# Optimization experiments

Measured on AMD Instinct MI355X. Metric: run time of the kernel, lower is better.

The kernel has to match this reference:

```python
import jax, jax.numpy as jnp
import numpy as np

EPS = 1e-8  # matches torch F.cosine_similarity default eps


def setup_inputs() -> dict:
    key = jax.random.key(0)
    k1, k2, k3 = jax.random.split(key, 3)
    B, S, Q, T, D = 1, 5, 512, 64, 2048
    supp = jax.random.normal(k1, (B, S, T, D), dtype=jnp.float32)
    query = jax.random.normal(k2, (B, Q, T, D), dtype=jnp.float32)
    query_ys = jax.random.randint(k3, (Q,), 0, S, dtype=jnp.int64)
    return {"supp": supp, "query": query, "query_ys": query_ys}


def reference(supp, query, query_ys):
    # supp: [B, S, T, D], query: [B, Q, T, D]
    # Pool once over T (mathematically identical to repeat-then-mean).
    sp = supp.mean(axis=-2)   # [B, S, D]
    qp = query.mean(axis=-2)  # [B, Q, D]
    # Pairwise cosine similarity over D -> [B, Q, S]
    num = jnp.einsum('bqd,bsd->bqs', qp, sp)
    qn = jnp.linalg.norm(qp, axis=-1)  # [B, Q]
    sn = jnp.linalg.norm(sp, axis=-1)  # [B, S]
    denom = jnp.maximum(qn[:, :, None] * sn[:, None, :], EPS)
    dist = (num / denom)[0]  # squeeze(0) -> [Q, S]
    # Cross-entropy over the num_supp (class) axis
    logp = jax.nn.log_softmax(dist, axis=-1)
    loss = -jnp.take_along_axis(logp, query_ys[:, None], axis=1).mean()
    return (loss, 1.0 - dist)
```

## Files before the change

### kernel.cpp

```cpp
#include <hip/hip_runtime.h>
#include <hip/hip_bf16.h>

#define S_DIM 5
#define Q_DIM 512
#define T_DIM 64
#define D_DIM 2048
#define EPS_CS 1e-8f

typedef float f32x4 __attribute__((ext_vector_type(4)));

#define WS_SP    0
#define WS_QP    10240
#define WS_NORMS 1058816
#define WS_NLL   1059336

__device__ __forceinline__ float wave_reduce_sum(float v) {
    #pragma unroll
    for (int off = 32; off > 0; off >>= 1)
        v += __shfl_down(v, off, 64);
    return v;
}

__global__ __launch_bounds__(512) void pool_kernel(
    const float* __restrict__ supp, const float* __restrict__ query,
    float* __restrict__ sp, float* __restrict__ qp, float* __restrict__ norms)
{
    const int b   = blockIdx.x;
    const int tid = threadIdx.x;

    const float* src = (b < S_DIM)
        ? supp  + (size_t)b * T_DIM * D_DIM
        : query + (size_t)(b - S_DIM) * T_DIM * D_DIM;
    float* dst = (b < S_DIM)
        ? sp + (size_t)b * D_DIM
        : qp + (size_t)(b - S_DIM) * D_DIM;

    const f32x4* base = (const f32x4*)src;

    f32x4 acc = {0.f, 0.f, 0.f, 0.f};
    #pragma unroll 16
    for (int t = 0; t < T_DIM; ++t) {
        f32x4 v = __builtin_nontemporal_load(&base[t * (D_DIM / 4) + tid]);
        acc += v;
    }
    const float inv = 1.0f / (float)T_DIM;
    acc *= inv;

    ((f32x4*)dst)[tid] = acc;

    float sq = acc.x * acc.x + acc.y * acc.y + acc.z * acc.z + acc.w * acc.w;
    float r = wave_reduce_sum(sq);

    __shared__ float lds[8];
    const int wave = tid >> 6, lane = tid & 63;
    if (lane == 0) lds[wave] = r;
    __syncthreads();
    if (tid == 0) {
        float tot = 0.f;
        #pragma unroll
        for (int w = 0; w < 8; ++w) tot += lds[w];
        norms[b] = sqrtf(tot);
    }
}

__global__ __launch_bounds__(512) void dot_kernel(
    const float* __restrict__ sp, const float* __restrict__ qp,
    const float* __restrict__ norms, const int* __restrict__ ys,
    float* __restrict__ out, float* __restrict__ nll)
{
    const int wave = threadIdx.x >> 6;
    const int lane = threadIdx.x & 63;
    const int q    = blockIdx.x * 8 + wave;

    const f32x4* qv4 = (const f32x4*)(qp + (size_t)q * D_DIM);

    float dots[S_DIM];
    #pragma unroll
    for (int s = 0; s < S_DIM; ++s) dots[s] = 0.f;

    #pragma unroll
    for (int i = 0; i < D_DIM / 4 / 64; ++i) {
        const int idx = lane + i * 64;
        f32x4 v = qv4[idx];
        #pragma unroll
        for (int s = 0; s < S_DIM; ++s) {
            f32x4 sv = ((const f32x4*)(sp + (size_t)s * D_DIM))[idx];
            dots[s] += v.x * sv.x + v.y * sv.y + v.z * sv.z + v.w * sv.w;
        }
    }

    #pragma unroll
    for (int s = 0; s < S_DIM; ++s)
        dots[s] = wave_reduce_sum(dots[s]);

    if (lane == 0) {
        const float qn = norms[S_DIM + q];
        float dist[S_DIM];
        #pragma unroll
        for (int s = 0; s < S_DIM; ++s) {
            float d = dots[s] / fmaxf(qn * norms[s], EPS_CS);
            dist[s] = d;
            out[1 + (size_t)q * S_DIM + s] = 1.0f - d;
        }
        float m = dist[0];
        #pragma unroll
        for (int s = 1; s < S_DIM; ++s) m = fmaxf(m, dist[s]);
        float sum = 0.f;
        #pragma unroll
        for (int s = 0; s < S_DIM; ++s) sum += expf(dist[s] - m);
        const float lse = m + logf(sum);

        int y = ys[q];
        if (y < 0) y = 0;
        if (y >= S_DIM) y = S_DIM - 1;
        nll[q] = lse - dist[y];
    }
}

__global__ __launch_bounds__(512) void loss_kernel(
    const float* __restrict__ nll, float* __restrict__ out)
{
    const int q = threadIdx.x;
    float r = wave_reduce_sum(nll[q]);
    __shared__ float lds[8];
    const int wave = q >> 6, lane = q & 63;
    if (lane == 0) lds[wave] = r;
    __syncthreads();
    if (q == 0) {
        float tot = 0.f;
        #pragma unroll
        for (int w = 0; w < 8; ++w) tot += lds[w];
        out[0] = tot * (1.0f / (float)Q_DIM);
    }
}

extern "C" void kernel_launch(void* const* d_in, const int* in_sizes, int n_in,
                              void* d_out, int out_size, void* d_ws, size_t ws_size,
                              hipStream_t stream) {
    const float* supp  = (const float*)d_in[0];
    const float* query = (const float*)d_in[1];
    const int*   ys    = (const int*)d_in[2];
    float* out = (float*)d_out;

    float* ws    = (float*)d_ws;
    float* sp    = ws + WS_SP;
    float* qp    = ws + WS_QP;
    float* norms = ws + WS_NORMS;
    float* nll   = ws + WS_NLL;

    pool_kernel<<<S_DIM + Q_DIM, 512, 0, stream>>>(supp, query, sp, qp, norms);
    dot_kernel<<<Q_DIM / 8, 512, 0, stream>>>(sp, qp, norms, ys, out, nll);
    loss_kernel<<<1, 512, 0, stream>>>(nll, out);
}
```

Baseline: 65.70 us.

## Fuse query pooling with cosine-similarity dot products and split support pooling

The query mean-pool and the per-query dot products/norms now run in one kernel, one block per query, so the pooled query vector never goes to workspace and the separate dot kernel is removed. Support pooling becomes its own kernel spread over 40 blocks, with time split across waves and combined in LDS, so it no longer sits behind a handful of slow blocks. Support norms are recomputed in every query block instead of being read back. Nontemporal loads are replaced by plain loads, and the 134MB stream is now read mostly by the fused kernel.

Measured after the change: 54.73 us. 1.2x faster.

```diff
diff --git a/kernel.cpp b/kernel.cpp
--- a/kernel.cpp
+++ b/kernel.cpp
@@ -9,10 +9,8 @@
 
 typedef float f32x4 __attribute__((ext_vector_type(4)));
 
-#define WS_SP    0
-#define WS_QP    10240
-#define WS_NORMS 1058816
-#define WS_NLL   1059336
+#define WS_SP  0
+#define WS_NLL 10240
 
 __device__ __forceinline__ float wave_reduce_sum(float v) {
     #pragma unroll
@@ -21,84 +19,88 @@
     return v;
 }
 
-__global__ __launch_bounds__(512) void pool_kernel(
-    const float* __restrict__ supp, const float* __restrict__ query,
-    float* __restrict__ sp, float* __restrict__ qp, float* __restrict__ norms)
+__device__ __forceinline__ float dot4(f32x4 a, f32x4 b) {
+    return a.x * b.x + a.y * b.y + a.z * b.z + a.w * b.w;
+}
+
+__global__ __launch_bounds__(512) void supp_pool_kernel(
+    const float* __restrict__ supp, float* __restrict__ sp)
 {
-    const int b   = blockIdx.x;
-    const int tid = threadIdx.x;
+    const int s    = blockIdx.x >> 3;
+    const int c    = blockIdx.x & 7;
+    const int tg   = threadIdx.x >> 6;
+    const int lane = threadIdx.x & 63;
+    const int slot = c * 64 + lane;
 
-    const float* src = (b < S_DIM)
-        ? supp  + (size_t)b * T_DIM * D_DIM
-        : query + (size_t)(b - S_DIM) * T_DIM * D_DIM;
-    float* dst = (b < S_DIM)
-        ? sp + (size_t)b * D_DIM
-        : qp + (size_t)(b - S_DIM) * D_DIM;
-
-    const f32x4* base = (const f32x4*)src;
+    const f32x4* base = (const f32x4*)(supp + (size_t)s * T_DIM * D_DIM);
 
     f32x4 acc = {0.f, 0.f, 0.f, 0.f};
-    #pragma unroll 16
-    for (int t = 0; t < T_DIM; ++t) {
-        f32x4 v = __builtin_nontemporal_load(&base[t * (D_DIM / 4) + tid]);
-        acc += v;
+    #pragma unroll
+    for (int i = 0; i < 8; ++i) {
+        const int t = tg * 8 + i;
+        acc += base[t * (D_DIM / 4) + slot];
     }
-    const float inv = 1.0f / (float)T_DIM;
-    acc *= inv;
 
-    ((f32x4*)dst)[tid] = acc;
-
-    float sq = acc.x * acc.x + acc.y * acc.y + acc.z * acc.z + acc.w * acc.w;
-    float r = wave_reduce_sum(sq);
-
-    __shared__ float lds[8];
-    const int wave = tid >> 6, lane = tid & 63;
-    if (lane == 0) lds[wave] = r;
+    __shared__ f32x4 lds[8][64];
+    lds[tg][lane] = acc;
     __syncthreads();
-    if (tid == 0) {
-        float tot = 0.f;
+    if (tg == 0) {
+        f32x4 tot = lds[0][lane];
         #pragma unroll
-        for (int w = 0; w < 8; ++w) tot += lds[w];
-        norms[b] = sqrtf(tot);
+        for (int w = 1; w < 8; ++w) tot += lds[w][lane];
+        tot *= (1.0f / (float)T_DIM);
+        ((f32x4*)(sp + (size_t)s * D_DIM))[slot] = tot;
     }
 }
 
-__global__ __launch_bounds__(512) void dot_kernel(
-    const float* __restrict__ sp, const float* __restrict__ qp,
-    const float* __restrict__ norms, const int* __restrict__ ys,
-    float* __restrict__ out, float* __restrict__ nll)
+__global__ __launch_bounds__(512) void query_fused_kernel(
+    const float* __restrict__ query, const float* __restrict__ sp,
+    const int* __restrict__ ys, float* __restrict__ out,
+    float* __restrict__ nll)
 {
-    const int wave = threadIdx.x >> 6;
-    const int lane = threadIdx.x & 63;
-    const int q    = blockIdx.x * 8 + wave;
+    const int q   = blockIdx.x;
+    const int tid = threadIdx.x;
+    const f32x4* base = (const f32x4*)(query + (size_t)q * T_DIM * D_DIM);
 
-    const f32x4* qv4 = (const f32x4*)(qp + (size_t)q * D_DIM);
+    f32x4 acc = {0.f, 0.f, 0.f, 0.f};
+    #pragma unroll 8
+    for (int t = 0; t < T_DIM; ++t)
+        acc += base[t * (D_DIM / 4) + tid];
+    acc *= (1.0f / (float)T_DIM);
 
-    float dots[S_DIM];
+    float vals[11];
+    vals[5] = dot4(acc, acc);
     #pragma unroll
-    for (int s = 0; s < S_DIM; ++s) dots[s] = 0.f;
-
-    #pragma unroll
-    for (int i = 0; i < D_DIM / 4 / 64; ++i) {
-        const int idx = lane + i * 64;
-        f32x4 v = qv4[idx];
-        #pragma unroll
-        for (int s = 0; s < S_DIM; ++s) {
-            f32x4 sv = ((const f32x4*)(sp + (size_t)s * D_DIM))[idx];
-            dots[s] += v.x * sv.x + v.y * sv.y + v.z * sv.z + v.w * sv.w;
-        }
+    for (int s = 0; s < S_DIM; ++s) {
+        f32x4 sv = ((const f32x4*)(sp + (size_t)s * D_DIM))[tid];
+        vals[s]     = dot4(acc, sv);
+        vals[6 + s] = dot4(sv, sv);
     }
 
+    __shared__ float lds[8][11];
+    const int wave = tid >> 6, lane = tid & 63;
     #pragma unroll
-    for (int s = 0; s < S_DIM; ++s)
-        dots[s] = wave_reduce_sum(dots[s]);
+    for (int k = 0; k < 11; ++k) {
+        float r = wave_reduce_sum(vals[k]);
+        if (lane == 0) lds[wave][k] = r;
+    }
+    __syncthreads();
 
-    if (lane == 0) {
-        const float qn = norms[S_DIM + q];
+    if (tid == 0) {
+        float tot[11];
+        #pragma unroll
+        for (int k = 0; k < 11; ++k) {
+            float t = 0.f;
+            #pragma unroll
+            for (int w = 0; w < 8; ++w) t += lds[w][k];
+            tot[k] = t;
+        }
+        const float qn = sqrtf(tot[5]);
         float dist[S_DIM];
         #pragma unroll
         for (int s = 0; s < S_DIM; ++s) {
-            float d = dots[s] / fmaxf(qn * norms[s], EPS_CS);
+            const float sn = sqrtf(tot[6 + s]);
+            const float d  = tot[s] / fmaxf(qn * sn, EPS_CS);
             dist[s] = d;
             out[1 + (size_t)q * S_DIM + s] = 1.0f - d;
         }
@@ -142,13 +144,11 @@
     const int*   ys    = (const int*)d_in[2];
     float* out = (float*)d_out;
 
-    float* ws    = (float*)d_ws;
-    float* sp    = ws + WS_SP;
-    float* qp    = ws + WS_QP;
-    float* norms = ws + WS_NORMS;
-    float* nll   = ws + WS_NLL;
+    float* ws  = (float*)d_ws;
+    float* sp  = ws + WS_SP;
+    float* nll = ws + WS_NLL;
 
-    pool_kernel<<<S_DIM + Q_DIM, 512, 0, stream>>>(supp, query, sp, qp, norms);
-    dot_kernel<<<Q_DIM / 8, 512, 0, stream>>>(sp, qp, norms, ys, out, nll);
+    supp_pool_kernel<<<S_DIM * 8, 512, 0, stream>>>(supp, sp);
+    query_fused_kernel<<<Q_DIM, 512, 0, stream>>>(query, sp, ys, out, nll);
     loss_kernel<<<1, 512, 0, stream>>>(nll, out);
 }
```
